# Kernel tuning notes

Measured on AMD Instinct MI355X. Metric: run time of the kernel, lower is better.

Reference implementation:

```python
import jax, jax.numpy as jnp
import numpy as np

DIM, M_DIM, FOURIER, KNN = 128, 16, 4, 32
EDGE_IN = 2 * FOURIER + 2 * DIM + 1  # 265


def silu(x):
    return x * jax.nn.sigmoid(x)


def setup_inputs() -> dict:
    key = jax.random.key(0)
    ks = jax.random.split(key, 12)
    b, n = 2, 4096

    def w(k, shape):
        return jax.random.normal(k, shape, dtype=jnp.float32) * 0.02

    return {
        "feats": jax.random.normal(ks[0], (b, n, DIM), dtype=jnp.float32),
        "coors": jax.random.normal(ks[1], (b, n, 3), dtype=jnp.float32) * 3.0,
        # edge_mlp: Linear(265, 530) -> SiLU -> Linear(530, 16) -> SiLU
        "We1": w(ks[2], (EDGE_IN, 2 * EDGE_IN)), "be1": jnp.zeros((2 * EDGE_IN,), jnp.float32),
        "We2": w(ks[3], (2 * EDGE_IN, M_DIM)), "be2": jnp.zeros((M_DIM,), jnp.float32),
        # coors_mlp: Linear(16, 64) -> SiLU -> Linear(64, 1)
        "Wc1": w(ks[4], (M_DIM, 4 * M_DIM)), "bc1": jnp.zeros((4 * M_DIM,), jnp.float32),
        "Wc2": w(ks[5], (4 * M_DIM, 1)), "bc2": jnp.zeros((1,), jnp.float32),
        # node_mlp: Linear(dim+16, 2*dim) -> SiLU -> Linear(2*dim, dim)
        "Wn1": w(ks[6], (DIM + M_DIM, 2 * DIM)), "bn1": jnp.zeros((2 * DIM,), jnp.float32),
        "Wn2": w(ks[7], (2 * DIM, DIM)), "bn2": jnp.zeros((DIM,), jnp.float32),
    }


def reference(feats, coors, We1, be1, We2, be2, Wc1, bc1, Wc2, bc2, Wn1, bn1, Wn2, bn2):
    b, n, d = feats.shape
    # pairwise relative coords and squared distance: (b, n, n, 3), (b, n, n)
    rel_coors = coors[:, :, None, :] - coors[:, None, :, :]
    rel_dist = jnp.sum(rel_coors ** 2, axis=-1)

    # k nearest neighbors (smallest distance)
    _, idx = jax.lax.top_k(-rel_dist, KNN)  # (b, n, K)
    rel_coors = jnp.take_along_axis(rel_coors, idx[..., None], axis=2)  # (b, n, K, 3)
    rel_dist = jnp.take_along_axis(rel_dist, idx, axis=2)[..., None]    # (b, n, K, 1)

    # fourier encode distance -> (b, n, K, 2*F + 1)
    scales = 2.0 ** jnp.arange(FOURIER, dtype=rel_dist.dtype)
    xs = rel_dist[..., None] / scales  # (b, n, K, 1, F)
    fe = jnp.concatenate([jnp.sin(xs), jnp.cos(xs), rel_dist[..., None]], axis=-1)
    rel_dist = fe.reshape(b, n, KNN, 2 * FOURIER + 1)

    bidx = jnp.arange(b)[:, None, None]
    feats_j = feats[bidx, idx]                                   # (b, n, K, d)
    feats_i = jnp.broadcast_to(feats[:, :, None, :], (b, n, KNN, d))

    edge_in = jnp.concatenate([feats_i, feats_j, rel_dist], axis=-1)  # (b, n, K, 265)
    m_ij = silu(silu(edge_in @ We1 + be1) @ We2 + be2)                # (b, n, K, m)

    coor_w = (silu(m_ij @ Wc1 + bc1) @ Wc2 + bc2)[..., 0]             # (b, n, K)
    coors_out = jnp.einsum('bij,bijc->bic', coor_w, rel_coors) + coors

    m_i = m_ij.sum(axis=2)                                            # (b, n, m)
    node_h = silu(jnp.concatenate([feats, m_i], axis=-1) @ Wn1 + bn1)
    node_out = node_h @ Wn2 + bn2 + feats
    return node_out, coors_out
```

## Files before the change

kernel.cpp:

```cpp
#include <hip/hip_runtime.h>
#include <hip/hip_bf16.h>
#include <stdint.h>

typedef __hip_bfloat16 bf16;

using sh8    = __attribute__((ext_vector_type(8)))  short;
using sh4    = __attribute__((ext_vector_type(4)))  short;
using us4    = __attribute__((ext_vector_type(4)))  unsigned short;
using f32x16 = __attribute__((ext_vector_type(16))) float;
using fx4    = __attribute__((ext_vector_type(4)))  float;
using i32x2  = __attribute__((ext_vector_type(2)))  int;

#define NN    4096
#define NODES 8192
#define DIM   128
#define MD    16
#define KNNK  32
#define H1N   530
#define CPAD  544
#define PROW  1088

#define OFF_W1AB 0
#define OFF_WE2A 8704
#define OFF_WC1A 17536
#define OFF_BE2  19584
#define OFF_BC1  19616
#define OFF_WC2  19744
#define OFF_BC2  19872
#define WIMG_SH  19880

__device__ __forceinline__ float b2f(bf16 x){ return __bfloat162float(x); }
__device__ __forceinline__ bf16  f2b(float x){ return __float2bfloat16(x); }
__device__ __forceinline__ float silu_f(float x){
    return x * __builtin_amdgcn_rcpf(1.f + __expf(-x));
}

__device__ __forceinline__ unsigned short f2us(float f){
    unsigned x = __float_as_uint(f);
    unsigned r = x + 0x7FFFu + ((x >> 16) & 1u);
    return (unsigned short)(r >> 16);
}
__device__ __forceinline__ float us2f(unsigned short u){
    return __uint_as_float(((unsigned)u) << 16);
}
__device__ __forceinline__ unsigned pkbf(float a, float b){
    __hip_bfloat162 v = __float22bfloat162_rn(make_float2(a, b));
    return *(unsigned*)&v;
}
__device__ __forceinline__ void plswap(unsigned &a, unsigned &b){
    i32x2 r = __builtin_amdgcn_permlane32_swap((int)a, (int)b, false, false);
    a = (unsigned)r[0]; b = (unsigned)r[1];
}
__device__ __forceinline__ sh8 mk8(unsigned a, unsigned b, unsigned c, unsigned d){
    union { unsigned u[4]; sh8 s; } x;
    x.u[0] = a; x.u[1] = b; x.u[2] = c; x.u[3] = d;
    return x.s;
}

struct Ptrs { const void* p[14]; int n[14]; };

__global__ __launch_bounds__(256) void detect_kernel(Ptrs ps, int* flags){
    int tn = blockIdx.x;
    const bf16* s = (const bf16*)ps.p[tn];
    int n = ps.n[tn]; if (n > 8192) n = 8192;
    int bad = 0;
    for (int i = threadIdx.x; i < n; i += 256){
        float v = b2f(s[i]);
        if (!(fabsf(v) <= 64.f)) bad = 1;
    }
    __shared__ int sbad;
    if (threadIdx.x == 0) sbad = 0;
    __syncthreads();
    if (bad) atomicOr(&sbad, 1);
    __syncthreads();
    if (threadIdx.x == 0) flags[tn] = sbad;
}

struct ConvTab {
    const void* src[14];
    int dstoff[14];
    int prefix[15];
};

__global__ __launch_bounds__(256) void convert_all(ConvTab tab,
                                                   const int* __restrict__ flags,
                                                   float* __restrict__ base){
    int gid = blockIdx.x * 256 + threadIdx.x;
    if (gid >= tab.prefix[14]) return;
    int tn = 0;
    #pragma unroll
    for (int k = 1; k < 14; ++k)
        if (gid >= tab.prefix[k]) tn = k;
    int local = gid - tab.prefix[tn];
    int f = flags[tn];
    float v = f ? ((const float*)tab.src[tn])[local]
                : b2f(((const bf16*)tab.src[tn])[local]);
    base[tab.dstoff[tn] + local] = v;
}

__global__ __launch_bounds__(256) void prep_kernel(
        const float* __restrict__ We1, const float* __restrict__ We2,
        const float* __restrict__ Wc1, const float* __restrict__ be2,
        const float* __restrict__ bc1, const float* __restrict__ Wc2,
        const float* __restrict__ bc2, const float* __restrict__ feats,
        unsigned short* __restrict__ gwimg,
        unsigned short* __restrict__ We1T,
        unsigned short* __restrict__ fBF){
    int gid = blockIdx.x * 256 + threadIdx.x;
    if (gid < 4352){
        int c = gid >> 3, f = gid & 7;
        gwimg[OFF_W1AB + gid] = (c < H1N) ? f2us(We1[(size_t)(256 + f) * H1N + c]) : 0;
    } else if (gid < 8704){
        int e = gid - 4352; int c = e >> 3, jj = e & 7;
        gwimg[OFF_W1AB + 4352 + e] =
            (jj == 0 && c < H1N) ? f2us(We1[(size_t)264 * H1N + c]) : 0;
    } else if (gid < 17536){
        int e = gid - 8704; int o = e / 552, c = e - o * 552;
        gwimg[OFF_WE2A + e] = (c < H1N) ? f2us(We2[(size_t)c * 16 + o]) : 0;
    } else if (gid < 19584){
        int e = gid - 17536; int u = e >> 5, k = e & 31;
        gwimg[OFF_WC1A + e] = (k < 16) ? f2us(Wc1[(size_t)k * 64 + u]) : 0;
    } else if (gid < 19600){
        ((float*)(gwimg + OFF_BE2))[gid - 19584] = be2[gid - 19584];
    } else if (gid < 19664){
        ((float*)(gwimg + OFF_BC1))[gid - 19600] = bc1[gid - 19600];
    } else if (gid < 19728){
        ((float*)(gwimg + OFF_WC2))[gid - 19664] = Wc2[gid - 19664];
    } else if (gid < 19732){
        int z = gid - 19728;
        ((float*)(gwimg + OFF_BC2))[z] = (z == 0) ? bc2[0] : 0.f;
    } else if (gid >= 32768 && gid < 32768 + 1088 * 128){
        int e = gid - 32768; int n = e >> 7, k = e & 127;
        float v;
        if (n < CPAD) v = (n < H1N) ? We1[(size_t)k * H1N + n] : 0.f;
        else { int n2 = n - CPAD; v = (n2 < H1N) ? We1[(size_t)(128 + k) * H1N + n2] : 0.f; }
        We1T[e] = f2us(v);
    } else if (gid >= 172032 && gid < 172032 + NODES * DIM){
        int e = gid - 172032;
        fBF[e] = f2us(feats[e]);
    }
}

__global__ __launch_bounds__(512, 6) void knn_kernel(const float* __restrict__ coors,
                                                     int* __restrict__ idx_out){
    __shared__ unsigned hist[8][1024];
    __shared__ unsigned long long blist[8][64];
    __shared__ int cntO[8], cntB[8];

    int t = threadIdx.x, lane = t & 63, wid = t >> 6;
    int node = (blockIdx.x << 3) + wid;
    int b = node >> 12, i = node & (NN - 1);
    const float* cb = coors + (size_t)b * NN * 3;

    float qx = cb[i*3+0], qy = cb[i*3+1], qz = cb[i*3+2];

    unsigned* h = &hist[wid][0];
    {
        uint4* hz = (uint4*)h;
        uint4 z = make_uint4(0,0,0,0);
        #pragma unroll
        for (int zl = 0; zl < 4; ++zl) hz[zl * 64 + lane] = z;
    }
    if (lane == 0){ cntO[wid] = 0; cntB[wid] = 0; }
    asm volatile("" ::: "memory");

    #pragma unroll 4
    for (int s = 0; s < 64; ++s){
        int j = (s << 6) + lane;
        float dx = qx - cb[j*3+0];
        float dy = qy - cb[j*3+1];
        float dz = qz - cb[j*3+2];
        float d  = dx*dx + dy*dy + dz*dz;
        float d2 = d * d;
        atomicAdd(&h[__float_as_uint(d2 * d2) >> 22], 1u);
    }
    asm volatile("s_waitcnt lgkmcnt(0)" ::: "memory");

    unsigned S = 0;
    {
        uint4* hz = (uint4*)h;
        #pragma unroll
        for (int g = 0; g < 4; ++g){
            uint4 v = hz[lane * 4 + g];
            S += v.x + v.y + v.z + v.w;
        }
    }
    unsigned scan = S;
    #pragma unroll
    for (int off = 1; off < 64; off <<= 1){
        unsigned nv = __shfl_up(scan, off);
        if (lane >= off) scan += nv;
    }
    unsigned excl = scan - S;
    unsigned long long own = __ballot(excl < KNNK && excl + S >= KNNK);
    int src = __ffsll((unsigned long long)own) - 1;
    unsigned run = excl, Bloc = 0, below_l = 0;
    #pragma unroll
    for (int r = 0; r < 16; ++r){
        unsigned c = h[lane * 16 + r];
        if (run < KNNK && run + c >= KNNK){ Bloc = lane * 16 + r; below_l = run; }
        run += c;
    }
    unsigned B    = __shfl(Bloc, src);
    unsigned below= __shfl(below_l, src);
    unsigned need = KNNK - below;

    int* co = &cntO[wid];
    int* cbn = &cntB[wid];
    unsigned long long* bl = &blist[wid][0];
    #pragma unroll 4
    for (int s = 0; s < 64; ++s){
        int j = (s << 6) + lane;
        float dx = qx - cb[j*3+0];
        float dy = qy - cb[j*3+1];
        float dz = qz - cb[j*3+2];
        float d  = dx*dx + dy*dy + dz*dz;
        float d2 = d * d;
        unsigned bk = __float_as_uint(d2 * d2) >> 22;
        if (bk < B){
            int pos = atomicAdd(co, 1);
            idx_out[(size_t)node * KNNK + pos] = j;
        } else if (bk == B){
            unsigned long long mk = ((unsigned long long)__float_as_uint(d) << 32)
                                    | (unsigned)j;
            int p = atomicAdd(cbn, 1);
            if (p < 64) bl[p] = mk;
        }
    }
    asm volatile("s_waitcnt lgkmcnt(0) vmcnt(0)" ::: "memory");
    int nb = *cbn;

    if (nb <= 64){
        unsigned long long e = (lane < nb) ? bl[lane] : ~0ull;
        for (unsigned r = 0; r < need; ++r){
            unsigned long long m = e;
            #pragma unroll
            for (int off = 32; off > 0; off >>= 1){
                unsigned long long o = __shfl_xor(m, off);
                if (o < m) m = o;
            }
            if (lane == 0)
                idx_out[(size_t)node * KNNK + below + r] = (int)(unsigned)(m & 0xffffffffull);
            if (e == m) e = ~0ull;
        }
    } else {
        unsigned long long lastk = 0;
        for (unsigned r = 0; r < need; ++r){
            unsigned long long lmin = ~0ull;
            for (int s = 0; s < 64; ++s){
                int j = (s << 6) + lane;
                float dx = qx - cb[j*3+0];
                float dy = qy - cb[j*3+1];
                float dz = qz - cb[j*3+2];
                float d  = dx*dx + dy*dy + dz*dz;
                float d2 = d * d;
                if ((__float_as_uint(d2 * d2) >> 22) == B){
                    unsigned long long mk = (((unsigned long long)__float_as_uint(d) << 32)
                                             | (unsigned)j) + 1ull;
                    if (mk > lastk && mk < lmin) lmin = mk;
                }
            }
            #pragma unroll
            for (int off = 32; off > 0; off >>= 1){
                unsigned long long o = __shfl_xor(lmin, off);
                if (o < lmin) lmin = o;
            }
            if (lane == 0)
                idx_out[(size_t)node * KNNK + below + r] =
                    (int)(unsigned)((lmin - 1ull) & 0xffffffffull);
            lastk = lmin;
        }
    }
}

__global__ __launch_bounds__(256) void p_gemm(const unsigned short* __restrict__ fBF,
                                              const unsigned short* __restrict__ We1T,
                                              const float* __restrict__ be1,
                                              unsigned short* __restrict__ P){
    int t = threadIdx.x, lane = t & 63, wid = t >> 6;
    int e31 = lane & 31, hi = lane >> 5;
    int mW = (blockIdx.x << 7) + (wid << 5);
    int n0 = blockIdx.y << 5;

    const unsigned short* Arow = fBF  + (size_t)(mW + e31) * DIM + hi * 8;
    const unsigned short* Brow = We1T + (size_t)(n0 + e31) * DIM + hi * 8;

    f32x16 acc = {0.f,0.f,0.f,0.f,0.f,0.f,0.f,0.f,0.f,0.f,0.f,0.f,0.f,0.f,0.f,0.f};
    #pragma unroll
    for (int kc = 0; kc < 8; ++kc){
        sh8 a  = *(const sh8*)(Arow + kc * 16);
        sh8 bv = *(const sh8*)(Brow + kc * 16);
        acc = __builtin_amdgcn_mfma_f32_32x32x16_bf16(a, bv, acc, 0, 0, 0);
    }
    int n = n0 + e31;
    float beadd = 0.f;
    if (n < CPAD) beadd = (n < H1N) ? be1[n] : 0.f;
    #pragma unroll
    for (int g = 0; g < 4; ++g)
        #pragma unroll
        for (int r = 0; r < 4; ++r){
            int m = mW + 8*g + 4*hi + r;
            P[(size_t)m * PROW + n] = f2us(acc[4*g + r] + beadd);
        }
}

__global__ __launch_bounds__(512, 6) void edge_kernel(
        const float* __restrict__ coors, const int* __restrict__ idx,
        const unsigned short* __restrict__ gw,
        const unsigned short* __restrict__ P,
        float* __restrict__ mi_out, void* __restrict__ dout,
        const int* __restrict__ flagp){
    __shared__ __align__(16) unsigned short sWe2[16 * 552];
    __shared__ __align__(16) unsigned short trans[8][1280];

    int t = threadIdx.x, lane = t & 63, wid = t >> 6;
    int gnode = (blockIdx.x << 3) + wid;
    int b = gnode >> 12;

    {
        const float4* s1 = (const float4*)(gw + OFF_WE2A);
        float4* d1 = (float4*)sWe2;
        for (int e = t; e < 1104; e += 512) d1[e] = s1[e];
    }

    const float* cb = coors + (size_t)b * NN * 3;
    int i = gnode & (NN - 1);
    float qx = cb[i*3+0], qy = cb[i*3+1], qz = cb[i*3+2];

    int e31 = lane & 31, hi = lane >> 5;
    int e15 = lane & 15, q  = lane >> 4;

    int jme = idx[(size_t)gnode * KNNK + e31];
    float rx = qx - cb[jme*3+0];
    float ry = qy - cb[jme*3+1];
    float rz = qz - cb[jme*3+2];
    float d = rx*rx + ry*ry + rz*rz;

    float s8v, c8v;
    __sincosf(d * 0.125f, &s8v, &c8v);
    float s4  = 2.f*s8v*c8v, c4  = 1.f - 2.f*s8v*s8v;
    float s2a = 2.f*s4*c4,   c2a = 1.f - 2.f*s4*s4;
    float s1a = 2.f*s2a*c2a, c1a = 1.f - 2.f*s2a*s2a;

    unsigned frb[9];
    frb[0] = f2us(s1a); frb[1] = f2us(s2a); frb[2] = f2us(s4); frb[3] = f2us(s8v);
    frb[4] = f2us(c1a); frb[5] = f2us(c2a); frb[6] = f2us(c4); frb[7] = f2us(c8v);
    frb[8] = f2us(d);

    sh8 bfragC;
    #pragma unroll
    for (int j = 0; j < 8; ++j)
        bfragC[j] = (hi == 0) ? (short)frb[j]
                  : (short)((j == 0) ? frb[8] : (j == 1) ? 0x3F80u : 0u);

    int nbase = gnode & ~(NN - 1);
    int j0 = __shfl(jme, lane >> 2);
    int j1 = __shfl(jme, 16 + (lane >> 2));
    const unsigned short* Pst0 = P + (size_t)(nbase + j0) * PROW + CPAD + (lane & 3) * 8;
    const unsigned short* Pst1 = P + (size_t)(nbase + j1) * PROW + CPAD + (lane & 3) * 8;
    const unsigned short* Pirow = P + (size_t)gnode * PROW;

    unsigned short* stg = &trans[wid][0];
    unsigned short* sw0 = stg + (lane >> 2) * 40 + (lane & 3) * 8;
    unsigned short* sw1 = stg + (16 + (lane >> 2)) * 40 + (lane & 3) * 8;

    const float* g_be2 = (const float*)(gw + OFF_BE2);
    const float* g_bc1 = (const float*)(gw + OFF_BC1);
    const float* g_wc2 = (const float*)(gw + OFF_WC2);
    const float* g_bc2 = (const float*)(gw + OFF_BC2);

    f32x16 accD = {0.f,0.f,0.f,0.f,0.f,0.f,0.f,0.f,
                   0.f,0.f,0.f,0.f,0.f,0.f,0.f,0.f};

    sh8 g0v = *(const sh8*)(Pst0);
    sh8 g1v = *(const sh8*)(Pst1);

    __syncthreads();

    #pragma unroll 1
    for (int ch = 0; ch < 17; ++ch){
        int c0 = ch * 32;
        *(sh8*)sw0 = g0v;
        *(sh8*)sw1 = g1v;
        if (ch < 16){
            g0v = *(const sh8*)(Pst0 + c0 + 32);
            g1v = *(const sh8*)(Pst1 + c0 + 32);
        }

        unsigned short piS = Pirow[c0 + e31];
        sh8 afrag = *(const sh8*)(gw + OFF_W1AB + (size_t)(hi * 544 + c0 + e31) * 8);
        afrag[1] = hi ? (short)piS : afrag[1];

        f32x16 cc;
        #pragma unroll
        for (int g = 0; g < 4; ++g){
            us4 pj = *(const us4*)(stg + e31 * 40 + 8*g + 4*hi);
            cc[4*g+0] = us2f(pj.x);
            cc[4*g+1] = us2f(pj.y);
            cc[4*g+2] = us2f(pj.z);
            cc[4*g+3] = us2f(pj.w);
        }
        f32x16 h = __builtin_amdgcn_mfma_f32_32x32x16_bf16(afrag, bfragC, cc, 0, 0, 0);

        unsigned u0 = pkbf(silu_f(h[0]),  silu_f(h[1]));
        unsigned u1 = pkbf(silu_f(h[2]),  silu_f(h[3]));
        unsigned u2 = pkbf(silu_f(h[4]),  silu_f(h[5]));
        unsigned u3 = pkbf(silu_f(h[6]),  silu_f(h[7]));
        unsigned u4 = pkbf(silu_f(h[8]),  silu_f(h[9]));
        unsigned u5 = pkbf(silu_f(h[10]), silu_f(h[11]));
        unsigned u6 = pkbf(silu_f(h[12]), silu_f(h[13]));
        unsigned u7 = pkbf(silu_f(h[14]), silu_f(h[15]));
        plswap(u0, u2); plswap(u1, u3);
        plswap(u4, u6); plswap(u5, u7);
        sh8 A1 = mk8(u0, u1, u2, u3);
        sh8 A2 = mk8(u4, u5, u6, u7);

        const unsigned short* wrow = &sWe2[(size_t)(e31 & 15) * 552 + c0 + (hi << 3)];
        sh8 B1 = *(const sh8*)(wrow);
        sh8 B2 = *(const sh8*)(wrow + 16);
        accD = __builtin_amdgcn_mfma_f32_32x32x16_bf16(A1, B1, accD, 0, 0, 0);
        accD = __builtin_amdgcn_mfma_f32_32x32x16_bf16(A2, B2, accD, 0, 0, 0);
    }

    float be2v = g_be2[e31 & 15];
    float mval[16];
    float msum = 0.f;
    #pragma unroll
    for (int r = 0; r < 16; ++r){
        mval[r] = silu_f(accD[r] + be2v);
        msum += mval[r];
    }
    msum += __shfl_xor(msum, 32);

    if (e31 < 16){
        #pragma unroll
        for (int r = 0; r < 16; ++r){
            int edge = (r & 3) + 8 * (r >> 2) + 4 * hi;
            stg[edge * 16 + e31] = f2us(mval[r]);
        }
        if (hi == 0)
            mi_out[(size_t)gnode * MD + e31] = msum;
    }

    float tsum0 = 0.f, tsum1 = 0.f;
    #pragma unroll
    for (int ut = 0; ut < 4; ++ut){
        sh8 wa3 = *(const sh8*)(gw + OFF_WC1A + (size_t)(ut * 16 + e15) * 32 + q * 8);
        sh8 b0  = (q < 2) ? *(const sh8*)&stg[e15 * 16 + q * 8]        : (sh8)0;
        sh8 b1  = (q < 2) ? *(const sh8*)&stg[(16 + e15) * 16 + q * 8] : (sh8)0;
        fx4 a0 = {0.f,0.f,0.f,0.f};
        fx4 a1 = {0.f,0.f,0.f,0.f};
        a0 = __builtin_amdgcn_mfma_f32_16x16x32_bf16(wa3, b0, a0, 0, 0, 0);
        a1 = __builtin_amdgcn_mfma_f32_16x16x32_bf16(wa3, b1, a1, 0, 0, 0);
        fx4 bc1q = *(const fx4*)&g_bc1[ut * 16 + q * 4];
        fx4 wcq  = *(const fx4*)&g_wc2[ut * 16 + q * 4];
        #pragma unroll
        for (int r = 0; r < 4; ++r){
            tsum0 += silu_f(a0[r] + bc1q[r]) * wcq[r];
            tsum1 += silu_f(a1[r] + bc1q[r]) * wcq[r];
        }
    }
    tsum0 += __shfl_xor(tsum0, 16); tsum0 += __shfl_xor(tsum0, 32);
    tsum1 += __shfl_xor(tsum1, 16); tsum1 += __shfl_xor(tsum1, 32);
    float cw = ((lane < 16) ? tsum0 : tsum1) + g_bc2[0];

    float en = (lane < 32) ? 1.f : 0.f;
    float cx = en * cw * rx, cy = en * cw * ry, cz = en * cw * rz;
    #pragma unroll
    for (int off = 1; off <= 32; off <<= 1){
        cx += __shfl_xor(cx, off);
        cy += __shfl_xor(cy, off);
        cz += __shfl_xor(cz, off);
    }
    if (lane == 0){
        size_t base = (size_t)NODES * DIM + (size_t)gnode * 3;
        if (*flagp){
            float* o = (float*)dout;
            o[base+0] = cx + qx; o[base+1] = cy + qy; o[base+2] = cz + qz;
        } else {
            bf16* o = (bf16*)dout;
            o[base+0] = f2b(cx + qx); o[base+1] = f2b(cy + qy); o[base+2] = f2b(cz + qz);
        }
    }
}

__global__ __launch_bounds__(256) void node_kernel(
        const float* __restrict__ feats, const float* __restrict__ m_i,
        const float* __restrict__ Wn1,   const float* __restrict__ bn1,
        const float* __restrict__ Wn2,   const float* __restrict__ bn2,
        void* __restrict__ dout,         const int* __restrict__ flagp){
    __shared__ float X[8][144];
    __shared__ float Hs[8][256];
    int t = threadIdx.x;
    int g0 = blockIdx.x << 3;

    for (int e = t; e < 8 * DIM; e += 256){
        int nd = e >> 7, c = e & 127;
        X[nd][c] = feats[(size_t)(g0 + nd) * DIM + c];
    }
    if (t < 128){
        int nd = t >> 4, c = t & 15;
        X[nd][DIM + c] = m_i[(size_t)(g0 + nd) * MD + c];
    }
    __syncthreads();

    float acc[8] = {};
    for (int r = 0; r < 144; ++r){
        float w = Wn1[(size_t)r * 256 + t];
        #pragma unroll
        for (int nd = 0; nd < 8; ++nd) acc[nd] += X[nd][r] * w;
    }
    float bb = bn1[t];
    #pragma unroll
    for (int nd = 0; nd < 8; ++nd) Hs[nd][t] = silu_f(acc[nd] + bb);
    __syncthreads();

    int c = t & 127, g = t >> 7;
    float a2[4] = {};
    for (int r = 0; r < 256; ++r){
        float w = Wn2[(size_t)r * DIM + c];
        #pragma unroll
        for (int u = 0; u < 4; ++u) a2[u] += Hs[g*4 + u][r] * w;
    }
    float b2v = bn2[c];
    int fl = *flagp;
    #pragma unroll
    for (int u = 0; u < 4; ++u){
        int nd = g*4 + u;
        float v = a2[u] + b2v + X[nd][c];
        size_t off2 = (size_t)(g0 + nd) * DIM + c;
        if (fl) ((float*)dout)[off2] = v;
        else    ((bf16*)dout)[off2]  = f2b(v);
    }
}

extern "C" void kernel_launch(void* const* d_in, const int* in_sizes, int n_in,
                              void* d_out, int out_size, void* d_ws, size_t ws_size,
                              hipStream_t stream){
    char* ws = (char*)d_ws;
    size_t off = 0;
    auto alloc = [&](size_t bytes) -> char* {
        off = (off + 511) & ~(size_t)511;
        char* p = ws + off;
        off += bytes;
        return p;
    };

    int* flags = (int*)alloc(14 * 4);

    ConvTab tab;
    int total = 0;
    for (int i = 0; i < 14; ++i){ tab.prefix[i] = total; total += in_sizes[i]; }
    tab.prefix[14] = total;
    float* convBase = (float*)alloc((size_t)total * 4);
    int doff = 0;
    for (int i = 0; i < 14; ++i){
        tab.src[i] = d_in[i];
        tab.dstoff[i] = doff;
        doff += in_sizes[i];
    }

    unsigned short* gwimg = (unsigned short*)alloc((size_t)WIMG_SH * 2);
    unsigned short* We1T  = (unsigned short*)alloc((size_t)1088 * 128 * 2);
    unsigned short* fBF   = (unsigned short*)alloc((size_t)NODES * DIM * 2);
    int*   idx    = (int*)  alloc((size_t)NODES * KNNK * 4);
    unsigned short* P = (unsigned short*) alloc((size_t)NODES * PROW * 2);
    float* mi     = (float*)alloc((size_t)NODES * MD * 4);

    Ptrs ps;
    for (int i = 0; i < 14; ++i){ ps.p[i] = d_in[i]; ps.n[i] = in_sizes[i]; }
    detect_kernel<<<14, 256, 0, stream>>>(ps, flags);
    convert_all<<<(total + 255) / 256, 256, 0, stream>>>(tab, flags, convBase);

    const float* feats = convBase + tab.dstoff[0];
    const float* coors = convBase + tab.dstoff[1];
    const float* We1 = convBase + tab.dstoff[2],  * be1 = convBase + tab.dstoff[3];
    const float* We2 = convBase + tab.dstoff[4],  * be2 = convBase + tab.dstoff[5];
    const float* Wc1 = convBase + tab.dstoff[6],  * bc1 = convBase + tab.dstoff[7];
    const float* Wc2 = convBase + tab.dstoff[8],  * bc2 = convBase + tab.dstoff[9];
    const float* Wn1 = convBase + tab.dstoff[10], * bn1 = convBase + tab.dstoff[11];
    const float* Wn2 = convBase + tab.dstoff[12], * bn2 = convBase + tab.dstoff[13];

    prep_kernel<<<(172032 + NODES * DIM) / 256, 256, 0, stream>>>(
        We1, We2, Wc1, be2, bc1, Wc2, bc2, feats, gwimg, We1T, fBF);
    knn_kernel<<<NODES/8, 512, 0, stream>>>(coors, idx);
    p_gemm<<<dim3(64, 34), 256, 0, stream>>>(fBF, We1T, be1, P);
    edge_kernel<<<NODES/8, 512, 0, stream>>>(coors, idx, gwimg, P, mi,
                                             d_out, flags + 0);
    node_kernel<<<1024, 256, 0, stream>>>(feats, mi, Wn1, bn1, Wn2, bn2,
                                          d_out, flags + 0);
}
```

Baseline: 252.5 us.

## Fold input conversion into prep kernel and co-schedule kNN with P GEMM

Drops the separate convert_all pass: prep_all now reads raw inputs (fp32 or bf16, chosen by the detected flag) and writes only the converted buffers later kernels need. The kNN kernel and the P projection GEMM are merged into one launch, with blocks interleaved so kNN blocks and GEMM blocks share the device at the same time. The GEMM tile per block doubles to 8 waves covering 64 output columns. This removes a kernel launch and a full conversion round-trip, and lets the MFMA-heavy GEMM overlap the latency-bound kNN search, at the cost of GEMM blocks being limited by the kNN kernel's launch bounds and shared-memory footprint.

```diff
diff --git a/kernel.cpp b/kernel.cpp
--- a/kernel.cpp
+++ b/kernel.cpp
@@ -56,6 +56,9 @@
     x.u[0] = a; x.u[1] = b; x.u[2] = c; x.u[3] = d;
     return x.s;
 }
+__device__ __forceinline__ float ldconv(const void* p, int fl, size_t i){
+    return fl ? ((const float*)p)[i] : b2f(((const bf16*)p)[i]);
+}
 
 struct Ptrs { const void* p[14]; int n[14]; };
 
@@ -76,79 +79,115 @@
     if (threadIdx.x == 0) flags[tn] = sbad;
 }
 
-struct ConvTab {
-    const void* src[14];
-    int dstoff[14];
-    int prefix[15];
-};
-
-__global__ __launch_bounds__(256) void convert_all(ConvTab tab,
-                                                   const int* __restrict__ flags,
-                                                   float* __restrict__ base){
-    int gid = blockIdx.x * 256 + threadIdx.x;
-    if (gid >= tab.prefix[14]) return;
-    int tn = 0;
-    #pragma unroll
-    for (int k = 1; k < 14; ++k)
-        if (gid >= tab.prefix[k]) tn = k;
-    int local = gid - tab.prefix[tn];
-    int f = flags[tn];
-    float v = f ? ((const float*)tab.src[tn])[local]
-                : b2f(((const bf16*)tab.src[tn])[local]);
-    base[tab.dstoff[tn] + local] = v;
-}
-
-__global__ __launch_bounds__(256) void prep_kernel(
-        const float* __restrict__ We1, const float* __restrict__ We2,
-        const float* __restrict__ Wc1, const float* __restrict__ be2,
-        const float* __restrict__ bc1, const float* __restrict__ Wc2,
-        const float* __restrict__ bc2, const float* __restrict__ feats,
-        unsigned short* __restrict__ gwimg,
-        unsigned short* __restrict__ We1T,
-        unsigned short* __restrict__ fBF){
+#define PREP_TOTAL 1315776
+__global__ __launch_bounds__(256) void prep_all(Ptrs ps, const int* __restrict__ flags,
+        unsigned short* __restrict__ gwimg, unsigned short* __restrict__ We1T,
+        unsigned short* __restrict__ fBF,   float* __restrict__ coorsF,
+        float* __restrict__ be1F,  float* __restrict__ Wn1F,
+        float* __restrict__ bn1F,  float* __restrict__ Wn2F,
+        float* __restrict__ bn2F){
     int gid = blockIdx.x * 256 + threadIdx.x;
     if (gid < 4352){
         int c = gid >> 3, f = gid & 7;
-        gwimg[OFF_W1AB + gid] = (c < H1N) ? f2us(We1[(size_t)(256 + f) * H1N + c]) : 0;
+        gwimg[OFF_W1AB + gid] =
+            (c < H1N) ? f2us(ldconv(ps.p[2], flags[2], (size_t)(256 + f) * H1N + c)) : 0;
     } else if (gid < 8704){
         int e = gid - 4352; int c = e >> 3, jj = e & 7;
         gwimg[OFF_W1AB + 4352 + e] =
-            (jj == 0 && c < H1N) ? f2us(We1[(size_t)264 * H1N + c]) : 0;
+            (jj == 0 && c < H1N) ? f2us(ldconv(ps.p[2], flags[2], (size_t)264 * H1N + c)) : 0;
     } else if (gid < 17536){
         int e = gid - 8704; int o = e / 552, c = e - o * 552;
-        gwimg[OFF_WE2A + e] = (c < H1N) ? f2us(We2[(size_t)c * 16 + o]) : 0;
+        gwimg[OFF_WE2A + e] =
+            (c < H1N) ? f2us(ldconv(ps.p[4], flags[4], (size_t)c * 16 + o)) : 0;
     } else if (gid < 19584){
         int e = gid - 17536; int u = e >> 5, k = e & 31;
-        gwimg[OFF_WC1A + e] = (k < 16) ? f2us(Wc1[(size_t)k * 64 + u]) : 0;
+        gwimg[OFF_WC1A + e] =
+            (k < 16) ? f2us(ldconv(ps.p[6], flags[6], (size_t)k * 64 + u)) : 0;
     } else if (gid < 19600){
-        ((float*)(gwimg + OFF_BE2))[gid - 19584] = be2[gid - 19584];
+        ((float*)(gwimg + OFF_BE2))[gid - 19584] = ldconv(ps.p[5], flags[5], gid - 19584);
     } else if (gid < 19664){
-        ((float*)(gwimg + OFF_BC1))[gid - 19600] = bc1[gid - 19600];
+        ((float*)(gwimg + OFF_BC1))[gid - 19600] = ldconv(ps.p[7], flags[7], gid - 19600);
     } else if (gid < 19728){
-        ((float*)(gwimg + OFF_WC2))[gid - 19664] = Wc2[gid - 19664];
+        ((float*)(gwimg + OFF_WC2))[gid - 19664] = ldconv(ps.p[8], flags[8], gid - 19664);
     } else if (gid < 19732){
         int z = gid - 19728;
-        ((float*)(gwimg + OFF_BC2))[z] = (z == 0) ? bc2[0] : 0.f;
-    } else if (gid >= 32768 && gid < 32768 + 1088 * 128){
+        ((float*)(gwimg + OFF_BC2))[z] = (z == 0) ? ldconv(ps.p[9], flags[9], 0) : 0.f;
+    } else if (gid >= 32768 && gid < 172032){
         int e = gid - 32768; int n = e >> 7, k = e & 127;
         float v;
-        if (n < CPAD) v = (n < H1N) ? We1[(size_t)k * H1N + n] : 0.f;
-        else { int n2 = n - CPAD; v = (n2 < H1N) ? We1[(size_t)(128 + k) * H1N + n2] : 0.f; }
+        if (n < CPAD) v = (n < H1N) ? ldconv(ps.p[2], flags[2], (size_t)k * H1N + n) : 0.f;
+        else { int n2 = n - CPAD;
+               v = (n2 < H1N) ? ldconv(ps.p[2], flags[2], (size_t)(128 + k) * H1N + n2) : 0.f; }
         We1T[e] = f2us(v);
-    } else if (gid >= 172032 && gid < 172032 + NODES * DIM){
+    } else if (gid >= 172032 && gid < 1220608){
         int e = gid - 172032;
-        fBF[e] = f2us(feats[e]);
-    }
-}
-
-__global__ __launch_bounds__(512, 6) void knn_kernel(const float* __restrict__ coors,
-                                                     int* __restrict__ idx_out){
+        fBF[e] = f2us(ldconv(ps.p[0], flags[0], e));
+    } else if (gid >= 1220608 && gid < 1245184){
+        int e = gid - 1220608;
+        coorsF[e] = ldconv(ps.p[1], flags[1], e);
+    } else if (gid >= 1245184 && gid < 1245714){
+        int e = gid - 1245184;
+        be1F[e] = ldconv(ps.p[3], flags[3], e);
+    } else if (gid >= 1245760 && gid < 1282624){
+        int e = gid - 1245760;
+        Wn1F[e] = ldconv(ps.p[10], flags[10], e);
+    } else if (gid >= 1282624 && gid < 1282880){
+        int e = gid - 1282624;
+        bn1F[e] = ldconv(ps.p[11], flags[11], e);
+    } else if (gid >= 1282880 && gid < 1315648){
+        int e = gid - 1282880;
+        Wn2F[e] = ldconv(ps.p[12], flags[12], e);
+    } else if (gid >= 1315648 && gid < 1315776){
+        int e = gid - 1315648;
+        bn2F[e] = ldconv(ps.p[13], flags[13], e);
+    }
+}
+
+__global__ __launch_bounds__(512, 6) void knn_pgemm(
+        const float* __restrict__ coors, int* __restrict__ idx_out,
+        const unsigned short* __restrict__ fBF,
+        const unsigned short* __restrict__ We1T,
+        const float* __restrict__ be1, unsigned short* __restrict__ P){
     __shared__ unsigned hist[8][1024];
     __shared__ unsigned long long blist[8][64];
     __shared__ int cntO[8], cntB[8];
 
+    int bid = blockIdx.x;
     int t = threadIdx.x, lane = t & 63, wid = t >> 6;
-    int node = (blockIdx.x << 3) + wid;
+    int e31 = lane & 31, hi = lane >> 5;
+
+    bool is_knn = (bid < 2048) && !(bid & 1);
+    int sub = (bid < 2048) ? (bid >> 1) : (bid - 1024);
+
+    if (!is_knn){
+        int bx = sub & 63, by = sub >> 6;
+        int mW = (bx << 7) + ((wid & 3) << 5);
+        int n0 = (by << 6) + ((wid >> 2) << 5);
+
+        const unsigned short* Arow = fBF  + (size_t)(mW + e31) * DIM + hi * 8;
+        const unsigned short* Brow = We1T + (size_t)(n0 + e31) * DIM + hi * 8;
+
+        f32x16 acc = {0.f,0.f,0.f,0.f,0.f,0.f,0.f,0.f,0.f,0.f,0.f,0.f,0.f,0.f,0.f,0.f};
+        #pragma unroll
+        for (int kc = 0; kc < 8; ++kc){
+            sh8 a  = *(const sh8*)(Arow + kc * 16);
+            sh8 bv = *(const sh8*)(Brow + kc * 16);
+            acc = __builtin_amdgcn_mfma_f32_32x32x16_bf16(a, bv, acc, 0, 0, 0);
+        }
+        int n = n0 + e31;
+        float beadd = 0.f;
+        if (n < CPAD) beadd = (n < H1N) ? be1[n] : 0.f;
+        #pragma unroll
+        for (int g = 0; g < 4; ++g)
+            #pragma unroll
+            for (int r = 0; r < 4; ++r){
+                int m = mW + 8*g + 4*hi + r;
+                P[(size_t)m * PROW + n] = f2us(acc[4*g + r] + beadd);
+            }
+        return;
+    }
+
+    int node = (sub << 3) + wid;
     int b = node >> 12, i = node & (NN - 1);
     const float* cb = coors + (size_t)b * NN * 3;
 
@@ -273,37 +312,6 @@
     }
 }
 
-__global__ __launch_bounds__(256) void p_gemm(const unsigned short* __restrict__ fBF,
-                                              const unsigned short* __restrict__ We1T,
-                                              const float* __restrict__ be1,
-                                              unsigned short* __restrict__ P){
-    int t = threadIdx.x, lane = t & 63, wid = t >> 6;
-    int e31 = lane & 31, hi = lane >> 5;
-    int mW = (blockIdx.x << 7) + (wid << 5);
-    int n0 = blockIdx.y << 5;
-
-    const unsigned short* Arow = fBF  + (size_t)(mW + e31) * DIM + hi * 8;
-    const unsigned short* Brow = We1T + (size_t)(n0 + e31) * DIM + hi * 8;
-
-    f32x16 acc = {0.f,0.f,0.f,0.f,0.f,0.f,0.f,0.f,0.f,0.f,0.f,0.f,0.f,0.f,0.f,0.f};
-    #pragma unroll
-    for (int kc = 0; kc < 8; ++kc){
-        sh8 a  = *(const sh8*)(Arow + kc * 16);
-        sh8 bv = *(const sh8*)(Brow + kc * 16);
-        acc = __builtin_amdgcn_mfma_f32_32x32x16_bf16(a, bv, acc, 0, 0, 0);
-    }
-    int n = n0 + e31;
-    float beadd = 0.f;
-    if (n < CPAD) beadd = (n < H1N) ? be1[n] : 0.f;
-    #pragma unroll
-    for (int g = 0; g < 4; ++g)
-        #pragma unroll
-        for (int r = 0; r < 4; ++r){
-            int m = mW + 8*g + 4*hi + r;
-            P[(size_t)m * PROW + n] = f2us(acc[4*g + r] + beadd);
-        }
-}
-
 __global__ __launch_bounds__(512, 6) void edge_kernel(
         const float* __restrict__ coors, const int* __restrict__ idx,
         const unsigned short* __restrict__ gw,
@@ -485,7 +493,7 @@
 }
 
 __global__ __launch_bounds__(256) void node_kernel(
-        const float* __restrict__ feats, const float* __restrict__ m_i,
+        const void* __restrict__ featsRaw, const float* __restrict__ m_i,
         const float* __restrict__ Wn1,   const float* __restrict__ bn1,
         const float* __restrict__ Wn2,   const float* __restrict__ bn2,
         void* __restrict__ dout,         const int* __restrict__ flagp){
@@ -493,10 +501,13 @@
     __shared__ float Hs[8][256];
     int t = threadIdx.x;
     int g0 = blockIdx.x << 3;
+    int fl = flagp[0];
 
     for (int e = t; e < 8 * DIM; e += 256){
         int nd = e >> 7, c = e & 127;
-        X[nd][c] = feats[(size_t)(g0 + nd) * DIM + c];
+        size_t off = (size_t)(g0 + nd) * DIM + c;
+        X[nd][c] = fl ? ((const float*)featsRaw)[off]
+                      : b2f(((const bf16*)featsRaw)[off]);
     }
     if (t < 128){
         int nd = t >> 4, c = t & 15;
@@ -523,7 +534,6 @@
         for (int u = 0; u < 4; ++u) a2[u] += Hs[g*4 + u][r] * w;
     }
     float b2v = bn2[c];
-    int fl = *flagp;
     #pragma unroll
     for (int u = 0; u < 4; ++u){
         int nd = g*4 + u;
@@ -547,46 +557,28 @@
     };
 
     int* flags = (int*)alloc(14 * 4);
-
-    ConvTab tab;
-    int total = 0;
-    for (int i = 0; i < 14; ++i){ tab.prefix[i] = total; total += in_sizes[i]; }
-    tab.prefix[14] = total;
-    float* convBase = (float*)alloc((size_t)total * 4);
-    int doff = 0;
-    for (int i = 0; i < 14; ++i){
-        tab.src[i] = d_in[i];
-        tab.dstoff[i] = doff;
-        doff += in_sizes[i];
-    }
-
     unsigned short* gwimg = (unsigned short*)alloc((size_t)WIMG_SH * 2);
     unsigned short* We1T  = (unsigned short*)alloc((size_t)1088 * 128 * 2);
     unsigned short* fBF   = (unsigned short*)alloc((size_t)NODES * DIM * 2);
+    float* coorsF = (float*)alloc((size_t)2 * NN * 3 * 4);
+    float* be1F   = (float*)alloc((size_t)544 * 4);
+    float* Wn1F   = (float*)alloc((size_t)144 * 256 * 4);
+    float* bn1F   = (float*)alloc((size_t)256 * 4);
+    float* Wn2F   = (float*)alloc((size_t)256 * 128 * 4);
+    float* bn2F   = (float*)alloc((size_t)128 * 4);
     int*   idx    = (int*)  alloc((size_t)NODES * KNNK * 4);
     unsigned short* P = (unsigned short*) alloc((size_t)NODES * PROW * 2);
     float* mi     = (float*)alloc((size_t)NODES * MD * 4);
 
     Ptrs ps;
     for (int i = 0; i < 14; ++i){ ps.p[i] = d_in[i]; ps.n[i] = in_sizes[i]; }
+
     detect_kernel<<<14, 256, 0, stream>>>(ps, flags);
-    convert_all<<<(total + 255) / 256, 256, 0, stream>>>(tab, flags, convBase);
-
-    const float* feats = convBase + tab.dstoff[0];
-    const float* coors = convBase + tab.dstoff[1];
-    const float* We1 = convBase + tab.dstoff[2],  * be1 = convBase + tab.dstoff[3];
-    const float* We2 = convBase + tab.dstoff[4],  * be2 = convBase + tab.dstoff[5];
-    const float* Wc1 = convBase + tab.dstoff[6],  * bc1 = convBase + tab.dstoff[7];
-    const float* Wc2 = convBase + tab.dstoff[8],  * bc2 = convBase + tab.dstoff[9];
-    const float* Wn1 = convBase + tab.dstoff[10], * bn1 = convBase + tab.dstoff[11];
-    const float* Wn2 = convBase + tab.dstoff[12], * bn2 = convBase + tab.dstoff[13];
-
-    prep_kernel<<<(172032 + NODES * DIM) / 256, 256, 0, stream>>>(
-        We1, We2, Wc1, be2, bc1, Wc2, bc2, feats, gwimg, We1T, fBF);
-    knn_kernel<<<NODES/8, 512, 0, stream>>>(coors, idx);
-    p_gemm<<<dim3(64, 34), 256, 0, stream>>>(fBF, We1T, be1, P);
-    edge_kernel<<<NODES/8, 512, 0, stream>>>(coors, idx, gwimg, P, mi,
+    prep_all<<<(PREP_TOTAL + 255) / 256, 256, 0, stream>>>(
+        ps, flags, gwimg, We1T, fBF, coorsF, be1F, Wn1F, bn1F, Wn2F, bn2F);
+    knn_pgemm<<<2112, 512, 0, stream>>>(coorsF, idx, fBF, We1T, be1F, P);
+    edge_kernel<<<NODES/8, 512, 0, stream>>>(coorsF, idx, gwimg, P, mi,
                                              d_out, flags + 0);
-    node_kernel<<<1024, 256, 0, stream>>>(feats, mi, Wn1, bn1, Wn2, bn2,
+    node_kernel<<<1024, 256, 0, stream>>>(d_in[0], mi, Wn1F, bn1F, Wn2F, bn2F,
                                           d_out, flags + 0);
 }
```

Measured after the change: 272.3 us. 1.08x slower.
